# Kernel tuning notes

Measured on AMD Instinct MI355X. Metric: run time of the kernel, lower is better.

The kernel has to match this reference:

```python
import jax, jax.numpy as jnp
import numpy as np

N_NODES = 100000    # nodes in river network
N_PATHS = 1000000   # number of (src, dst) routing paths
MAX_DELAY = 16
DT = 1.0
CASCADE = 1.0
T = int(MAX_DELAY / DT)        # expanded time window (assert in original)
E = 8000000                    # total flattened path-node entries


def setup_inputs() -> dict:
    key = jax.random.key(0)
    k1, k2, k3 = jax.random.split(key, 3)
    params = jax.random.uniform(k1, (N_NODES,), dtype=jnp.float32)
    path_idxs = jnp.sort(jax.random.randint(k2, (E,), 0, N_PATHS, dtype=jnp.int32))
    path_nodes = jax.random.randint(k3, (E,), 0, N_NODES, dtype=jnp.int32)
    return {"params": params, "path_idxs": path_idxs, "path_nodes": path_nodes}


def reference(params, path_idxs, path_nodes):
    # irf_fn 'linear_storage': per-node linear-reservoir impulse response h(t)=exp(-t/k)/k
    k = params + 0.5                                  # storage const in [0.5, 1.5)
    t = jnp.arange(T, dtype=params.dtype) * DT        # [T]
    irfs = jnp.exp(-t[None, :] / k[:, None]) / k[:, None]   # [N, T]
    # frequency domain
    irfs_freq = jnp.fft.rfft(irfs, n=T, axis=-1)      # [N, F] complex
    # irf_agg 'log_triton': cascade-combine IRFs along each path = product of
    # transfer functions, done in log domain: gather logs, segment-sum per path.
    log_freq = jnp.log(irfs_freq)                     # [N, F] complex log
    gathered = log_freq[path_nodes]                   # [E, F] irregular gather
    agg_re = jax.ops.segment_sum(gathered.real, path_idxs, num_segments=N_PATHS)
    agg_im = jax.ops.segment_sum(gathered.imag, path_idxs, num_segments=N_PATHS)
    agg_log = (agg_re + 1j * agg_im) * CASCADE        # [P, F]
    irfs_freq_agg = jnp.exp(agg_log)
    # back to time domain
    irfs_agg = jnp.fft.irfft(irfs_freq_agg, n=T, axis=-1)   # [P, T]
    irfs_agg = jax.nn.relu(irfs_agg)
    irfs_agg = jnp.flip(irfs_agg, -1)                 # sampler.phi_k is identity for dt=1
    irfs_agg = irfs_agg / jnp.sum(irfs_agg, -1, keepdims=True)
    return irfs_agg                                   # COO values; coords scatter is a storage step
```

## Files before the change

kernel.cpp:

```cpp
#include <hip/hip_runtime.h>
#include <math.h>

#define N_NODES  100000
#define N_PATHS  1000000
#define E_TOT    8000000
#define NW_TOT   (E_TOT / 4)
#define TAB_U32  25000
#define EB       1024
#define EPT      8
#define PB       256
#define KW       9

#define RMIN 0.135330f
#define RMAX 0.513420f
#define QSCALE (255.0f / (RMAX - RMIN))
#define DEQ    ((RMAX - RMIN) / 255.0f)

typedef int   v4i __attribute__((ext_vector_type(4)));
typedef float v4f __attribute__((ext_vector_type(4)));
typedef unsigned long long u64;

__device__ __constant__ float COS16[16] = {
  1.0f,  0.92387953f,  0.70710678f,  0.38268343f,  0.0f, -0.38268343f, -0.70710678f, -0.92387953f,
 -1.0f, -0.92387953f, -0.70710678f, -0.38268343f,  0.0f,  0.38268343f,  0.70710678f,  0.92387953f };
__device__ __constant__ float SIN16[16] = {
  0.0f,  0.38268343f,  0.70710678f,  0.92387953f,  1.0f,  0.92387953f,  0.70710678f,  0.38268343f,
  0.0f, -0.38268343f, -0.70710678f, -0.92387953f, -1.0f, -0.92387953f, -0.70710678f, -0.38268343f };

__global__ void node_rq_kernel(const float* __restrict__ params,
                               unsigned char* __restrict__ rtab_q) {
    int n = blockIdx.x * blockDim.x + threadIdx.x;
    if (n >= N_NODES) return;
    float k = params[n] + 0.5f;
    float r = expf(-1.0f / k);
    float q = (r - RMIN) * QSCALE;
    q = fminf(fmaxf(q + 0.5f, 0.0f), 255.0f);
    rtab_q[n] = (unsigned char)q;
}

__device__ __forceinline__ void put_bounds(int a, int b, int e, int* __restrict__ start) {
    for (int p = a + 1; p <= b; ++p) start[p] = e;
}

__global__ __launch_bounds__(EB) void epass_kernel(const int* __restrict__ pidx,
                                                   const int* __restrict__ pnode,
                                                   const unsigned int* __restrict__ rtab_q,
                                                   int* __restrict__ start,
                                                   unsigned char* __restrict__ r8_all) {
    __shared__ v4i tab4[TAB_U32 / 4];
    const unsigned char* tabb = (const unsigned char*)tab4;
    int tid = threadIdx.x;
    int base_q = blockIdx.x * (EB * EPT);

    if (base_q + EB * EPT <= NW_TOT) {
        const v4i* pidx4  = (const v4i*)pidx;
        const v4i* pnode4 = (const v4i*)pnode;

        v4i va[4], wa[4];
#pragma unroll
        for (int g = 0; g < 4; ++g) {
            va[g] = pidx4[base_q + g * EB + tid];
            wa[g] = pnode4[base_q + g * EB + tid];
        }
        int wbase = tid & ~63;
        int qpf = base_q + (tid & 7) * EB + wbase;
        int apf = 4 * qpf - 1;
        int pp = pidx[apf < 0 ? 0 : apf];
        for (int i = tid; i < TAB_U32 / 4; i += EB)
            tab4[i] = ((const v4i*)rtab_q)[i];
        __syncthreads();

        v4i vb[4], wb[4];
#pragma unroll
        for (int g = 0; g < 4; ++g) {
            vb[g] = pidx4[base_q + (g + 4) * EB + tid];
            wb[g] = pnode4[base_q + (g + 4) * EB + tid];
        }

#pragma unroll
        for (int g = 0; g < 8; ++g) {
            v4i v = (g < 4) ? va[g & 3] : vb[g & 3];
            v4i w = (g < 4) ? wa[g & 3] : wb[g & 3];
            int q = base_q + g * EB + tid;
            int e = q * 4;
            uchar4 r;
            r.x = tabb[w.x];
            r.y = tabb[w.y];
            r.z = tabb[w.z];
            r.w = tabb[w.w];
            ((uchar4*)r8_all)[q] = r;
            int prev0 = __shfl(pp, g);
            int prev = __shfl_up((int)v.w, 1);
            if ((tid & 63) == 0) prev = (e == 0) ? -1 : prev0;
            put_bounds(prev, v.x, e,     start);
            put_bounds(v.x,  v.y, e + 1, start);
            put_bounds(v.y,  v.z, e + 2, start);
            put_bounds(v.z,  v.w, e + 3, start);
        }
    } else {
        for (int i = tid; i < TAB_U32; i += EB)
            ((unsigned int*)tab4)[i] = rtab_q[i];
        __syncthreads();
#pragma unroll
        for (int g = 0; g < EPT; g++) {
            int q = base_q + g * EB + tid;
            if (q >= NW_TOT) break;
            int e = q * 4;
            v4i v = *((const v4i*)pidx + q);
            v4i w = *((const v4i*)pnode + q);
            uchar4 r;
            r.x = tabb[w.x];
            r.y = tabb[w.y];
            r.z = tabb[w.z];
            r.w = tabb[w.w];
            ((uchar4*)r8_all)[q] = r;
            int prev = __shfl_up((int)v.w, 1);
            if ((tid & 63) == 0) prev = (e == 0) ? -1 : pidx[e - 1];
            put_bounds(prev, v.x, e,     start);
            put_bounds(v.x,  v.y, e + 1, start);
            put_bounds(v.y,  v.z, e + 2, start);
            put_bounds(v.z,  v.w, e + 3, start);
            if (e + 4 == E_TOT) {
                for (int p = v.w + 1; p <= N_PATHS; ++p) start[p] = E_TOT;
            }
        }
    }
}

__device__ __forceinline__ void quad_step(unsigned grp, int rem,
                                          float& d0, float& d8,
                                          float dr[7], float di[7]) {
    float ra = fmaf((float)(grp & 255u), DEQ, RMIN);
    float rb = (rem > 1) ? fmaf((float)((grp >> 8) & 255u), DEQ, RMIN) : 0.0f;
    float rc = (rem > 2) ? fmaf((float)((grp >> 16) & 255u), DEQ, RMIN) : 0.0f;
    float rd = (rem > 3) ? fmaf((float)(grp >> 24), DEQ, RMIN) : 0.0f;
    float sab = ra + rb, qab = ra * rb;
    float scd = rc + rd, qcd = rc * rd;
    float e1 = sab + scd;
    float e2 = fmaf(sab, scd, qab + qcd);
    float e3 = fmaf(qab, scd, qcd * sab);
    float e4 = qab * qcd;
#pragma unroll
    for (int f = 1; f <= 7; f++) {
        float tr = fmaf(-e1, COS16[f], 1.0f);
        tr = fmaf( e2, COS16[(2 * f) & 15], tr);
        tr = fmaf(-e3, COS16[(3 * f) & 15], tr);
        tr = fmaf( e4, COS16[(4 * f) & 15], tr);
        float ti = e1 * SIN16[f];
        ti = fmaf(-e2, SIN16[(2 * f) & 15], ti);
        ti = fmaf( e3, SIN16[(3 * f) & 15], ti);
        ti = fmaf(-e4, SIN16[(4 * f) & 15], ti);
        float a = dr[f - 1], b = di[f - 1];
        dr[f - 1] = fmaf(a, tr, -b * ti);
        di[f - 1] = fmaf(a, ti,  b * tr);
    }
    d0 *= ((1.0f - e1) + (e2 - e3)) + e4;
    d8 *= ((1.0f + e1) + (e2 + e3)) + e4;
}

__global__ __launch_bounds__(PB) void path_kernel(const int* __restrict__ start,
                                                  const unsigned int* __restrict__ r8w,
                                                  float* __restrict__ out) {
    __shared__ v4f lds_o[PB * 4];
    int tid = threadIdx.x;
    int p = blockIdx.x * PB + tid;
    int L = tid & 63;
    v4f* lw = lds_o + (tid >> 6) * 256;

    if (p < N_PATHS) {
        int s0 = start[p];
        int s1 = start[p + 1];
        int len = s1 - s0;
        int nq = (len + 3) >> 2;
        int a0 = s0 >> 2;
        unsigned sh = (unsigned)(s0 & 3) * 8u;

        unsigned wv[KW];
#pragma unroll
        for (int i = 0; i < KW; ++i) {
            int idx = a0 + i;
            wv[i] = r8w[idx < NW_TOT ? idx : (NW_TOT - 1)];
        }

        float d0 = 1.0f, d8 = 1.0f;
        float dr[7], di[7];
#pragma unroll
        for (int f = 0; f < 7; f++) { dr[f] = 1.0f; di[f] = 0.0f; }

#pragma unroll
        for (int q = 0; q < KW - 1; ++q) {
            if (q < nq) {
                unsigned grp = (unsigned)((((u64)wv[q + 1] << 32) |
                                           (u64)wv[q]) >> sh);
                quad_step(grp, len - 4 * q, d0, d8, dr, di);
            }
        }
        if (len > 32) {
            unsigned cur = wv[KW - 1];
            for (int q = KW - 1; q < nq; ++q) {
                int w = a0 + q + 1;
                unsigned nxt = (w < NW_TOT) ? r8w[w] : 0u;
                unsigned grp = (unsigned)((((u64)nxt << 32) | (u64)cur) >> sh);
                cur = nxt;
                quad_step(grp, len - 4 * q, d0, d8, dr, di);
            }
        }

        float Xr[8], Xi[8];
        Xr[0] = 1.0f; Xi[0] = 0.0f;
#pragma unroll
        for (int f = 1; f < 8; f++) {
            float a = dr[f - 1], b = di[f - 1];
            float m = fmaf(a, a, b * b);
            float inv = d0 * __builtin_amdgcn_rcpf(m);
            Xr[f] =  a * inv;
            Xi[f] = -b * inv;
        }
        float X8 = d0 * __builtin_amdgcn_rcpf(d8);

        float xt[16];
        float c0 = 0.0f, c8s = 0.0f;
#pragma unroll
        for (int f = 1; f < 8; f++) {
            c0 += 2.0f * Xr[f];
            c8s += (f & 1) ? -2.0f * Xr[f] : 2.0f * Xr[f];
        }
        xt[0] = fmaxf((Xr[0] + X8 + c0) * (1.0f / 16.0f), 0.0f);
        xt[8] = fmaxf((Xr[0] + X8 + c8s) * (1.0f / 16.0f), 0.0f);
        float ssum = xt[0] + xt[8];
#pragma unroll
        for (int t = 1; t < 8; t++) {
            float Ct = 0.0f, St = 0.0f;
#pragma unroll
            for (int f = 1; f < 8; f++) {
                int kk = (f * t) & 15;
                Ct = fmaf(2.0f * Xr[f], COS16[kk], Ct);
                St = fmaf(2.0f * Xi[f], SIN16[kk], St);
            }
            float base = Xr[0] + ((t & 1) ? -X8 : X8) + Ct;
            float xa = fmaxf((base - St) * (1.0f / 16.0f), 0.0f);
            float xb = fmaxf((base + St) * (1.0f / 16.0f), 0.0f);
            xt[t] = xa;
            xt[16 - t] = xb;
            ssum += xa + xb;
        }

        float invs = __builtin_amdgcn_rcpf(ssum);
        lw[L * 4 + (0 ^ (L & 3))] =
            (v4f){ xt[15] * invs, xt[14] * invs, xt[13] * invs, xt[12] * invs };
        lw[L * 4 + (1 ^ (L & 3))] =
            (v4f){ xt[11] * invs, xt[10] * invs, xt[9]  * invs, xt[8]  * invs };
        lw[L * 4 + (2 ^ (L & 3))] =
            (v4f){ xt[7]  * invs, xt[6]  * invs, xt[5]  * invs, xt[4]  * invs };
        lw[L * 4 + (3 ^ (L & 3))] =
            (v4f){ xt[3]  * invs, xt[2]  * invs, xt[1]  * invs, xt[0]  * invs };
    }

    __syncthreads();

    int P0 = (blockIdx.x * PB) + (tid & ~63);
    if (P0 < N_PATHS) {
        v4f* outw = (v4f*)out + (size_t)P0 * 4;
#pragma unroll
        for (int k = 0; k < 4; ++k) {
            int m = k * 64 + L;
            int q = m >> 2;
            int c = m & 3;
            outw[m] = lw[q * 4 + (c ^ (q & 3))];
        }
    }
}

extern "C" void kernel_launch(void* const* d_in, const int* in_sizes, int n_in,
                              void* d_out, int out_size, void* d_ws, size_t ws_size,
                              hipStream_t stream) {
    const float* params = (const float*)d_in[0];
    const int* path_idxs = (const int*)d_in[1];
    const int* path_nodes = (const int*)d_in[2];
    float* out = (float*)d_out;

    size_t off_rq    = 0;
    size_t off_start = (off_rq + (size_t)N_NODES + 1023) & ~(size_t)1023;
    size_t off_r8    = (off_start + (size_t)(N_PATHS + 1) * 4 + 1023) & ~(size_t)1023;

    unsigned char* rtab_q = (unsigned char*)d_ws + off_rq;
    int* start = (int*)((char*)d_ws + off_start);
    unsigned char* r8_all = (unsigned char*)d_ws + off_r8;

    {
        int threads = 256;
        int blocks = (N_NODES + threads - 1) / threads;
        node_rq_kernel<<<blocks, threads, 0, stream>>>(params, rtab_q);
    }
    {
        int per_block = EB * EPT;
        int blocks = (NW_TOT + per_block - 1) / per_block;
        epass_kernel<<<blocks, EB, 0, stream>>>(path_idxs, path_nodes,
                                                (const unsigned int*)rtab_q,
                                                start, r8_all);
    }
    {
        int blocks = (N_PATHS + PB - 1) / PB;
        path_kernel<<<blocks, PB, 0, stream>>>(start, (const unsigned int*)r8_all, out);
    }
}
```

Baseline: 136.7 us.

## Fuse edge pass and per-path compute into one kernel using LDS-resident codes

Merges the edge pass (quantized-code gather and segment-bound writes) with the per-path frequency-domain compute. Each block keeps its 32K quantized codes in LDS and directly evaluates the paths that lie fully inside its edge chunk. Paths spanning a chunk boundary are recorded via an atomic counter and finished by a small cleanup kernel that reads from global memory. This removes the separate path kernel launch and the global re-read of codes and start offsets. In exchange it adds per-block boundary logic, a threadfence, a cleanup launch and a fixed cap on the number of spanning paths.

```diff
diff --git a/kernel.cpp b/kernel.cpp
--- a/kernel.cpp
+++ b/kernel.cpp
@@ -6,10 +6,14 @@
 #define E_TOT    8000000
 #define NW_TOT   (E_TOT / 4)
 #define TAB_U32  25000
-#define EB       1024
-#define EPT      8
+#define FB       1024
+#define FPT      8
+#define ENT      (FB * FPT * 4)
+#define NBLK     ((E_TOT + ENT - 1) / ENT)
 #define PB       256
 #define KW       9
+#define CLEAN_MAX 8192
+#define R8OFF    100352
 
 #define RMIN 0.135330f
 #define RMAX 0.513420f
@@ -28,8 +32,10 @@
   0.0f, -0.38268343f, -0.70710678f, -0.92387953f, -1.0f, -0.92387953f, -0.70710678f, -0.38268343f };
 
 __global__ void node_rq_kernel(const float* __restrict__ params,
-                               unsigned char* __restrict__ rtab_q) {
+                               unsigned char* __restrict__ rtab_q,
+                               int* __restrict__ ccnt) {
     int n = blockIdx.x * blockDim.x + threadIdx.x;
+    if (n == 0) *ccnt = 0;
     if (n >= N_NODES) return;
     float k = params[n] + 0.5f;
     float r = expf(-1.0f / k);
@@ -40,91 +46,6 @@
 
 __device__ __forceinline__ void put_bounds(int a, int b, int e, int* __restrict__ start) {
     for (int p = a + 1; p <= b; ++p) start[p] = e;
-}
-
-__global__ __launch_bounds__(EB) void epass_kernel(const int* __restrict__ pidx,
-                                                   const int* __restrict__ pnode,
-                                                   const unsigned int* __restrict__ rtab_q,
-                                                   int* __restrict__ start,
-                                                   unsigned char* __restrict__ r8_all) {
-    __shared__ v4i tab4[TAB_U32 / 4];
-    const unsigned char* tabb = (const unsigned char*)tab4;
-    int tid = threadIdx.x;
-    int base_q = blockIdx.x * (EB * EPT);
-
-    if (base_q + EB * EPT <= NW_TOT) {
-        const v4i* pidx4  = (const v4i*)pidx;
-        const v4i* pnode4 = (const v4i*)pnode;
-
-        v4i va[4], wa[4];
-#pragma unroll
-        for (int g = 0; g < 4; ++g) {
-            va[g] = pidx4[base_q + g * EB + tid];
-            wa[g] = pnode4[base_q + g * EB + tid];
-        }
-        int wbase = tid & ~63;
-        int qpf = base_q + (tid & 7) * EB + wbase;
-        int apf = 4 * qpf - 1;
-        int pp = pidx[apf < 0 ? 0 : apf];
-        for (int i = tid; i < TAB_U32 / 4; i += EB)
-            tab4[i] = ((const v4i*)rtab_q)[i];
-        __syncthreads();
-
-        v4i vb[4], wb[4];
-#pragma unroll
-        for (int g = 0; g < 4; ++g) {
-            vb[g] = pidx4[base_q + (g + 4) * EB + tid];
-            wb[g] = pnode4[base_q + (g + 4) * EB + tid];
-        }
-
-#pragma unroll
-        for (int g = 0; g < 8; ++g) {
-            v4i v = (g < 4) ? va[g & 3] : vb[g & 3];
-            v4i w = (g < 4) ? wa[g & 3] : wb[g & 3];
-            int q = base_q + g * EB + tid;
-            int e = q * 4;
-            uchar4 r;
-            r.x = tabb[w.x];
-            r.y = tabb[w.y];
-            r.z = tabb[w.z];
-            r.w = tabb[w.w];
-            ((uchar4*)r8_all)[q] = r;
-            int prev0 = __shfl(pp, g);
-            int prev = __shfl_up((int)v.w, 1);
-            if ((tid & 63) == 0) prev = (e == 0) ? -1 : prev0;
-            put_bounds(prev, v.x, e,     start);
-            put_bounds(v.x,  v.y, e + 1, start);
-            put_bounds(v.y,  v.z, e + 2, start);
-            put_bounds(v.z,  v.w, e + 3, start);
-        }
-    } else {
-        for (int i = tid; i < TAB_U32; i += EB)
-            ((unsigned int*)tab4)[i] = rtab_q[i];
-        __syncthreads();
-#pragma unroll
-        for (int g = 0; g < EPT; g++) {
-            int q = base_q + g * EB + tid;
-            if (q >= NW_TOT) break;
-            int e = q * 4;
-            v4i v = *((const v4i*)pidx + q);
-            v4i w = *((const v4i*)pnode + q);
-            uchar4 r;
-            r.x = tabb[w.x];
-            r.y = tabb[w.y];
-            r.z = tabb[w.z];
-            r.w = tabb[w.w];
-            ((uchar4*)r8_all)[q] = r;
-            int prev = __shfl_up((int)v.w, 1);
-            if ((tid & 63) == 0) prev = (e == 0) ? -1 : pidx[e - 1];
-            put_bounds(prev, v.x, e,     start);
-            put_bounds(v.x,  v.y, e + 1, start);
-            put_bounds(v.y,  v.z, e + 2, start);
-            put_bounds(v.z,  v.w, e + 3, start);
-            if (e + 4 == E_TOT) {
-                for (int p = v.w + 1; p <= N_PATHS; ++p) start[p] = E_TOT;
-            }
-        }
-    }
 }
 
 __device__ __forceinline__ void quad_step(unsigned grp, int rem,
@@ -158,28 +79,177 @@
     d8 *= ((1.0f + e1) + (e2 + e3)) + e4;
 }
 
-__global__ __launch_bounds__(PB) void path_kernel(const int* __restrict__ start,
-                                                  const unsigned int* __restrict__ r8w,
-                                                  float* __restrict__ out) {
-    __shared__ v4f lds_o[PB * 4];
+__device__ __forceinline__ void epilogue16(float d0, float d8,
+                                           const float dr[7], const float di[7],
+                                           v4f o[4]) {
+    float Xr[8], Xi[8];
+    Xr[0] = 1.0f; Xi[0] = 0.0f;
+#pragma unroll
+    for (int f = 1; f < 8; f++) {
+        float a = dr[f - 1], b = di[f - 1];
+        float m = fmaf(a, a, b * b);
+        float inv = d0 * __builtin_amdgcn_rcpf(m);
+        Xr[f] =  a * inv;
+        Xi[f] = -b * inv;
+    }
+    float X8 = d0 * __builtin_amdgcn_rcpf(d8);
+
+    float xt[16];
+    float c0 = 0.0f, c8s = 0.0f;
+#pragma unroll
+    for (int f = 1; f < 8; f++) {
+        c0 += 2.0f * Xr[f];
+        c8s += (f & 1) ? -2.0f * Xr[f] : 2.0f * Xr[f];
+    }
+    xt[0] = fmaxf((Xr[0] + X8 + c0) * (1.0f / 16.0f), 0.0f);
+    xt[8] = fmaxf((Xr[0] + X8 + c8s) * (1.0f / 16.0f), 0.0f);
+    float ssum = xt[0] + xt[8];
+#pragma unroll
+    for (int t = 1; t < 8; t++) {
+        float Ct = 0.0f, St = 0.0f;
+#pragma unroll
+        for (int f = 1; f < 8; f++) {
+            int kk = (f * t) & 15;
+            Ct = fmaf(2.0f * Xr[f], COS16[kk], Ct);
+            St = fmaf(2.0f * Xi[f], SIN16[kk], St);
+        }
+        float base = Xr[0] + ((t & 1) ? -X8 : X8) + Ct;
+        float xa = fmaxf((base - St) * (1.0f / 16.0f), 0.0f);
+        float xb = fmaxf((base + St) * (1.0f / 16.0f), 0.0f);
+        xt[t] = xa;
+        xt[16 - t] = xb;
+        ssum += xa + xb;
+    }
+    float invs = __builtin_amdgcn_rcpf(ssum);
+    o[0] = (v4f){ xt[15] * invs, xt[14] * invs, xt[13] * invs, xt[12] * invs };
+    o[1] = (v4f){ xt[11] * invs, xt[10] * invs, xt[9]  * invs, xt[8]  * invs };
+    o[2] = (v4f){ xt[7]  * invs, xt[6]  * invs, xt[5]  * invs, xt[4]  * invs };
+    o[3] = (v4f){ xt[3]  * invs, xt[2]  * invs, xt[1]  * invs, xt[0]  * invs };
+}
+
+__global__ __launch_bounds__(FB) void fused_kernel(const int* __restrict__ pidx,
+                                                   const int* __restrict__ pnode,
+                                                   const unsigned int* __restrict__ rtab_q,
+                                                   int* __restrict__ start,
+                                                   unsigned int* __restrict__ r8_all,
+                                                   float* __restrict__ out,
+                                                   int* __restrict__ ccnt,
+                                                   int* __restrict__ clist) {
+    __shared__ v4i smem4[8320];
+    unsigned char* tabb = (unsigned char*)smem4;
+    unsigned int*  r8l  = (unsigned int*)(tabb + R8OFF);
+    v4f* stage = (v4f*)smem4;
+
     int tid = threadIdx.x;
-    int p = blockIdx.x * PB + tid;
+    int base_e = blockIdx.x * ENT;
+    int base_q = base_e >> 2;
+    int E1 = base_e + ENT; if (E1 > E_TOT) E1 = E_TOT;
+    bool lastb = (blockIdx.x == NBLK - 1);
+
+    int pprev = (base_e == 0) ? -1 : pidx[base_e - 1];
+    int plast = pidx[E1 - 1];
+    int peek  = lastb ? N_PATHS : pidx[E1];
+    bool spanning = (!lastb) && (peek == plast);
+    int SL = lastb ? (N_PATHS - 1) : (spanning ? plast - 1 : plast);
+
+    if (base_q + FB * FPT <= NW_TOT) {
+        const v4i* pidx4  = (const v4i*)pidx;
+        const v4i* pnode4 = (const v4i*)pnode;
+        v4i va[4], wa[4];
+#pragma unroll
+        for (int g = 0; g < 4; ++g) {
+            va[g] = pidx4[base_q + g * FB + tid];
+            wa[g] = pnode4[base_q + g * FB + tid];
+        }
+        int wbase = tid & ~63;
+        int qpf = base_q + (tid & 7) * FB + wbase;
+        int apf = 4 * qpf - 1;
+        int pp = pidx[apf < 0 ? 0 : apf];
+        for (int i = tid; i < TAB_U32 / 4; i += FB)
+            smem4[i] = ((const v4i*)rtab_q)[i];
+        __syncthreads();
+
+        v4i vb[4], wb[4];
+#pragma unroll
+        for (int g = 0; g < 4; ++g) {
+            vb[g] = pidx4[base_q + (g + 4) * FB + tid];
+            wb[g] = pnode4[base_q + (g + 4) * FB + tid];
+        }
+#pragma unroll
+        for (int g = 0; g < 8; ++g) {
+            v4i v = (g < 4) ? va[g & 3] : vb[g & 3];
+            v4i w = (g < 4) ? wa[g & 3] : wb[g & 3];
+            int q = base_q + g * FB + tid;
+            int e = q * 4;
+            unsigned rw = (unsigned)tabb[w.x] | ((unsigned)tabb[w.y] << 8) |
+                          ((unsigned)tabb[w.z] << 16) | ((unsigned)tabb[w.w] << 24);
+            r8_all[q] = rw;
+            r8l[g * FB + tid] = rw;
+            int prev0 = __shfl(pp, g);
+            int prev = __shfl_up((int)v.w, 1);
+            if ((tid & 63) == 0) prev = (e == 0) ? -1 : prev0;
+            put_bounds(prev, v.x, e,     start);
+            put_bounds(v.x,  v.y, e + 1, start);
+            put_bounds(v.y,  v.z, e + 2, start);
+            put_bounds(v.z,  v.w, e + 3, start);
+        }
+    } else {
+        for (int i = tid; i < TAB_U32 / 4; i += FB)
+            smem4[i] = ((const v4i*)rtab_q)[i];
+        __syncthreads();
+#pragma unroll
+        for (int g = 0; g < FPT; g++) {
+            int q = base_q + g * FB + tid;
+            if (q < NW_TOT) {
+                v4i v = *((const v4i*)pidx + q);
+                v4i w = *((const v4i*)pnode + q);
+                int e = q * 4;
+                unsigned rw = (unsigned)tabb[w.x] | ((unsigned)tabb[w.y] << 8) |
+                              ((unsigned)tabb[w.z] << 16) | ((unsigned)tabb[w.w] << 24);
+                r8_all[q] = rw;
+                r8l[q - base_q] = rw;
+                int prev = __shfl_up((int)v.w, 1);
+                if ((tid & 63) == 0) prev = (e == 0) ? -1 : pidx[e - 1];
+                put_bounds(prev, v.x, e,     start);
+                put_bounds(v.x,  v.y, e + 1, start);
+                put_bounds(v.y,  v.z, e + 2, start);
+                put_bounds(v.z,  v.w, e + 3, start);
+                if (e + 4 == E_TOT) {
+                    for (int p = v.w + 1; p <= N_PATHS; ++p) start[p] = E_TOT;
+                }
+            }
+        }
+    }
+
+    __threadfence();
+    __syncthreads();
+
+    if (spanning && tid == 0) {
+        int ix = atomicAdd(ccnt, 1);
+        if (ix < CLEAN_MAX) clist[ix] = plast;
+    }
+
+    int count = SL - pprev;
+    int rounds = (count + FB - 1) >> 10;
     int L = tid & 63;
-    v4f* lw = lds_o + (tid >> 6) * 256;
-
-    if (p < N_PATHS) {
-        int s0 = start[p];
-        int s1 = start[p + 1];
+    v4f* lw = stage + (tid >> 6) * 256;
+
+    for (int rr = 0; rr < rounds; ++rr) {
+        int p = pprev + 1 + (rr << 10) + tid;
+        int pc = (p <= SL) ? p : SL;
+        int s0 = start[pc];
+        int s1 = (pc == plast) ? E1 : start[pc + 1];
         int len = s1 - s0;
         int nq = (len + 3) >> 2;
-        int a0 = s0 >> 2;
-        unsigned sh = (unsigned)(s0 & 3) * 8u;
+        int lb = s0 - base_e;
+        int a0 = lb >> 2;
+        unsigned sh = (unsigned)(lb & 3) * 8u;
 
         unsigned wv[KW];
 #pragma unroll
         for (int i = 0; i < KW; ++i) {
             int idx = a0 + i;
-            wv[i] = r8w[idx < NW_TOT ? idx : (NW_TOT - 1)];
+            wv[i] = r8l[idx < (ENT / 4) ? idx : (ENT / 4 - 1)];
         }
 
         float d0 = 1.0f, d8 = 1.0f;
@@ -198,77 +268,81 @@
         if (len > 32) {
             unsigned cur = wv[KW - 1];
             for (int q = KW - 1; q < nq; ++q) {
-                int w = a0 + q + 1;
-                unsigned nxt = (w < NW_TOT) ? r8w[w] : 0u;
+                int widx = a0 + q + 1;
+                unsigned nxt = r8l[widx < (ENT / 4) ? widx : (ENT / 4 - 1)];
                 unsigned grp = (unsigned)((((u64)nxt << 32) | (u64)cur) >> sh);
                 cur = nxt;
                 quad_step(grp, len - 4 * q, d0, d8, dr, di);
             }
         }
 
-        float Xr[8], Xi[8];
-        Xr[0] = 1.0f; Xi[0] = 0.0f;
-#pragma unroll
-        for (int f = 1; f < 8; f++) {
-            float a = dr[f - 1], b = di[f - 1];
-            float m = fmaf(a, a, b * b);
-            float inv = d0 * __builtin_amdgcn_rcpf(m);
-            Xr[f] =  a * inv;
-            Xi[f] = -b * inv;
-        }
-        float X8 = d0 * __builtin_amdgcn_rcpf(d8);
-
-        float xt[16];
-        float c0 = 0.0f, c8s = 0.0f;
-#pragma unroll
-        for (int f = 1; f < 8; f++) {
-            c0 += 2.0f * Xr[f];
-            c8s += (f & 1) ? -2.0f * Xr[f] : 2.0f * Xr[f];
-        }
-        xt[0] = fmaxf((Xr[0] + X8 + c0) * (1.0f / 16.0f), 0.0f);
-        xt[8] = fmaxf((Xr[0] + X8 + c8s) * (1.0f / 16.0f), 0.0f);
-        float ssum = xt[0] + xt[8];
-#pragma unroll
-        for (int t = 1; t < 8; t++) {
-            float Ct = 0.0f, St = 0.0f;
-#pragma unroll
-            for (int f = 1; f < 8; f++) {
-                int kk = (f * t) & 15;
-                Ct = fmaf(2.0f * Xr[f], COS16[kk], Ct);
-                St = fmaf(2.0f * Xi[f], SIN16[kk], St);
-            }
-            float base = Xr[0] + ((t & 1) ? -X8 : X8) + Ct;
-            float xa = fmaxf((base - St) * (1.0f / 16.0f), 0.0f);
-            float xb = fmaxf((base + St) * (1.0f / 16.0f), 0.0f);
-            xt[t] = xa;
-            xt[16 - t] = xb;
-            ssum += xa + xb;
-        }
-
-        float invs = __builtin_amdgcn_rcpf(ssum);
-        lw[L * 4 + (0 ^ (L & 3))] =
-            (v4f){ xt[15] * invs, xt[14] * invs, xt[13] * invs, xt[12] * invs };
-        lw[L * 4 + (1 ^ (L & 3))] =
-            (v4f){ xt[11] * invs, xt[10] * invs, xt[9]  * invs, xt[8]  * invs };
-        lw[L * 4 + (2 ^ (L & 3))] =
-            (v4f){ xt[7]  * invs, xt[6]  * invs, xt[5]  * invs, xt[4]  * invs };
-        lw[L * 4 + (3 ^ (L & 3))] =
-            (v4f){ xt[3]  * invs, xt[2]  * invs, xt[1]  * invs, xt[0]  * invs };
-    }
-
-    __syncthreads();
-
-    int P0 = (blockIdx.x * PB) + (tid & ~63);
-    if (P0 < N_PATHS) {
-        v4f* outw = (v4f*)out + (size_t)P0 * 4;
+        v4f o[4];
+        epilogue16(d0, d8, dr, di, o);
+
+        lw[L * 4 + (0 ^ (L & 3))] = o[0];
+        lw[L * 4 + (1 ^ (L & 3))] = o[1];
+        lw[L * 4 + (2 ^ (L & 3))] = o[2];
+        lw[L * 4 + (3 ^ (L & 3))] = o[3];
+        int wvbase = pprev + 1 + (rr << 10) + (tid & ~63);
+        v4f* outw = (v4f*)out + (size_t)wvbase * 4;
 #pragma unroll
         for (int k = 0; k < 4; ++k) {
             int m = k * 64 + L;
-            int q = m >> 2;
-            int c = m & 3;
-            outw[m] = lw[q * 4 + (c ^ (q & 3))];
-        }
-    }
+            int ps = wvbase + (m >> 2);
+            if (ps <= SL)
+                outw[m] = lw[(m >> 2) * 4 + ((m & 3) ^ ((m >> 2) & 3))];
+        }
+    }
+}
+
+__global__ __launch_bounds__(PB) void cleanup_kernel(const int* __restrict__ ccnt,
+                                                     const int* __restrict__ clist,
+                                                     const int* __restrict__ start,
+                                                     const unsigned int* __restrict__ r8w,
+                                                     float* __restrict__ out) {
+    int t = blockIdx.x * PB + threadIdx.x;
+    int n = *ccnt; if (n > CLEAN_MAX) n = CLEAN_MAX;
+    if (t >= n) return;
+    int p = clist[t];
+
+    int s0 = start[p];
+    int s1 = start[p + 1];
+    int len = s1 - s0;
+    int nq = (len + 3) >> 2;
+    int a0 = s0 >> 2;
+    unsigned sh = (unsigned)(s0 & 3) * 8u;
+
+    unsigned wv[KW];
+#pragma unroll
+    for (int i = 0; i < KW; ++i) {
+        int idx = a0 + i;
+        wv[i] = r8w[idx < NW_TOT ? idx : (NW_TOT - 1)];
+    }
+    float d0 = 1.0f, d8 = 1.0f;
+    float dr[7], di[7];
+#pragma unroll
+    for (int f = 0; f < 7; f++) { dr[f] = 1.0f; di[f] = 0.0f; }
+#pragma unroll
+    for (int q = 0; q < KW - 1; ++q) {
+        if (q < nq) {
+            unsigned grp = (unsigned)((((u64)wv[q + 1] << 32) | (u64)wv[q]) >> sh);
+            quad_step(grp, len - 4 * q, d0, d8, dr, di);
+        }
+    }
+    if (len > 32) {
+        unsigned cur = wv[KW - 1];
+        for (int q = KW - 1; q < nq; ++q) {
+            int w = a0 + q + 1;
+            unsigned nxt = (w < NW_TOT) ? r8w[w] : 0u;
+            unsigned grp = (unsigned)((((u64)nxt << 32) | (u64)cur) >> sh);
+            cur = nxt;
+            quad_step(grp, len - 4 * q, d0, d8, dr, di);
+        }
+    }
+    v4f o[4];
+    epilogue16(d0, d8, dr, di, o);
+    v4f* op4 = (v4f*)(out + (size_t)p * 16);
+    op4[0] = o[0]; op4[1] = o[1]; op4[2] = o[2]; op4[3] = o[3];
 }
 
 extern "C" void kernel_launch(void* const* d_in, const int* in_sizes, int n_in,
@@ -282,25 +356,27 @@
     size_t off_rq    = 0;
     size_t off_start = (off_rq + (size_t)N_NODES + 1023) & ~(size_t)1023;
     size_t off_r8    = (off_start + (size_t)(N_PATHS + 1) * 4 + 1023) & ~(size_t)1023;
+    size_t off_cc    = (off_r8 + (size_t)E_TOT + 1023) & ~(size_t)1023;
+    size_t off_cl    = (off_cc + 1024) & ~(size_t)1023;
 
     unsigned char* rtab_q = (unsigned char*)d_ws + off_rq;
     int* start = (int*)((char*)d_ws + off_start);
-    unsigned char* r8_all = (unsigned char*)d_ws + off_r8;
+    unsigned int* r8_all = (unsigned int*)((char*)d_ws + off_r8);
+    int* ccnt = (int*)((char*)d_ws + off_cc);
+    int* clist = (int*)((char*)d_ws + off_cl);
 
     {
         int threads = 256;
         int blocks = (N_NODES + threads - 1) / threads;
-        node_rq_kernel<<<blocks, threads, 0, stream>>>(params, rtab_q);
+        node_rq_kernel<<<blocks, threads, 0, stream>>>(params, rtab_q, ccnt);
     }
     {
-        int per_block = EB * EPT;
-        int blocks = (NW_TOT + per_block - 1) / per_block;
-        epass_kernel<<<blocks, EB, 0, stream>>>(path_idxs, path_nodes,
-                                                (const unsigned int*)rtab_q,
-                                                start, r8_all);
+        fused_kernel<<<NBLK, FB, 0, stream>>>(path_idxs, path_nodes,
+                                              (const unsigned int*)rtab_q,
+                                              start, r8_all, out, ccnt, clist);
     }
     {
-        int blocks = (N_PATHS + PB - 1) / PB;
-        path_kernel<<<blocks, PB, 0, stream>>>(start, (const unsigned int*)r8_all, out);
-    }
-}
+        cleanup_kernel<<<CLEAN_MAX / PB, PB, 0, stream>>>(ccnt, clist, start,
+                                                          r8_all, out);
+    }
+}
```

After: 299.6 us. 119% more time.
